# Kernel tuning notes

Measured on AMD Instinct MI355X. Metric: run time of the kernel, lower is better.

Reference implementation:

```python
import jax, jax.numpy as jnp
import numpy as np

A_DIM, V_DIM, L_DIM, H = 512, 768, 1024, 512
B, S = 16, 2048


def setup_inputs() -> dict:
    key = jax.random.key(0)
    ks = jax.random.split(key, 20)
    w = lambda k, shp: jax.random.normal(k, shp, dtype=jnp.float32) * 0.02
    return {
        "a_input": jax.random.normal(ks[0], (B, S, A_DIM), dtype=jnp.float32),
        "v_input": jax.random.normal(ks[1], (B, S, V_DIM), dtype=jnp.float32),
        "l_input": jax.random.normal(ks[2], (B, S, L_DIM), dtype=jnp.float32),
        "h0": jax.random.normal(ks[3], (1, B, H), dtype=jnp.float32),
        "c0": jax.random.normal(ks[4], (1, B, H), dtype=jnp.float32),
        # 1x1 Conv1d == per-timestep Linear: weight [H, in_dim], bias [H]
        "Wa": w(ks[5], (H, A_DIM)), "ba": w(ks[6], (H,)),
        "Wv": w(ks[7], (H, V_DIM)), "bv": w(ks[8], (H,)),
        "Wl": w(ks[9], (H, L_DIM)), "bl": w(ks[10], (H,)),
        "Wc": w(ks[11], (H, 3 * H)), "bc": w(ks[12], (H,)),
        # LSTM params, PyTorch gate order (i, f, g, o)
        "Wih": w(ks[13], (4 * H, H)), "Whh": w(ks[14], (4 * H, H)),
        "bih": w(ks[15], (4 * H,)), "bhh": w(ks[16], (4 * H,)),
    }


def _lstm(x, h0, c0, Wih, Whh, bih, bhh):
    # x: [B, S, H]; h0/c0: [B, H]
    def step(carry, xt):
        h, c = carry
        gates = xt @ Wih.T + bih + h @ Whh.T + bhh  # [B, 4H]
        i, f, g, o = jnp.split(gates, 4, axis=-1)
        c = jax.nn.sigmoid(f) * c + jax.nn.sigmoid(i) * jnp.tanh(g)
        h = jax.nn.sigmoid(o) * jnp.tanh(c)
        return (h, c), h
    (hT, cT), hs = jax.lax.scan(step, (h0, c0), x.transpose(1, 0, 2))
    return hs.transpose(1, 0, 2), hT, cT  # [B,S,H], [B,H], [B,H]


def reference(a_input, v_input, l_input, h0, c0, Wa, ba, Wv, bv, Wl, bl,
              Wc, bc, Wih, Whh, bih, bhh):
    # 1x1 conv projections -> [B, S, H]
    a = a_input @ Wa.T + ba
    v = v_input @ Wv.T + bv
    l = l_input @ Wl.T + bl
    # attention fusion
    context = jnp.tanh(jnp.concatenate([a, v, l], axis=-1) @ Wc.T + bc)  # [B,S,H]
    scores = jnp.stack([
        jnp.sum(a * context, axis=-1),
        jnp.sum(v * context, axis=-1),
        jnp.sum(l * context, axis=-1),
    ], axis=-1)  # [B, S, 3]
    weight = jax.nn.softmax(scores, axis=-1)[..., None]  # [B,S,3,1]
    data = jnp.stack([a, v, l], axis=-2)  # [B,S,3,H]
    fusion = jnp.sum(data * weight, axis=-2)  # [B,S,H]
    r_out, hT, cT = _lstm(fusion, h0[0], c0[0], Wih, Whh, bih, bhh)
    return r_out, hT[None], cT[None]
```

## Files before the change

kernel.cpp:

```cpp
#include <hip/hip_runtime.h>
#include <stdint.h>

#define B_ 16
#define S_ 2048
#define H_ 512
#define M_ (B_ * S_)

template <int ACT>
__global__ __launch_bounds__(256) void gemm_xwt(
    const float* __restrict__ X, const float* __restrict__ W,
    const float* __restrict__ b1, const float* __restrict__ b2,
    float* __restrict__ Y, int K, int ldy)
{
  __shared__ float As[16][132];
  __shared__ float Bs[16][132];
  const int tid = threadIdx.x;
  const int bm = blockIdx.x, bn = blockIdx.y;
  const int ty = tid >> 4, tx = tid & 15;
  const int lr = tid >> 2, lk = (tid & 3) << 2;
  const float* Xb = X + (size_t)(bm * 128) * K;
  const float* Wb = W + (size_t)(bn * 128) * K;

  float acc[8][8] = {};

  for (int k0 = 0; k0 < K; k0 += 16) {
    float4 xa0 = *(const float4*)(Xb + (size_t)lr * K + k0 + lk);
    float4 xa1 = *(const float4*)(Xb + (size_t)(lr + 64) * K + k0 + lk);
    float4 wa0 = *(const float4*)(Wb + (size_t)lr * K + k0 + lk);
    float4 wa1 = *(const float4*)(Wb + (size_t)(lr + 64) * K + k0 + lk);
    __syncthreads();
    As[lk + 0][lr] = xa0.x; As[lk + 1][lr] = xa0.y; As[lk + 2][lr] = xa0.z; As[lk + 3][lr] = xa0.w;
    As[lk + 0][lr + 64] = xa1.x; As[lk + 1][lr + 64] = xa1.y; As[lk + 2][lr + 64] = xa1.z; As[lk + 3][lr + 64] = xa1.w;
    Bs[lk + 0][lr] = wa0.x; Bs[lk + 1][lr] = wa0.y; Bs[lk + 2][lr] = wa0.z; Bs[lk + 3][lr] = wa0.w;
    Bs[lk + 0][lr + 64] = wa1.x; Bs[lk + 1][lr + 64] = wa1.y; Bs[lk + 2][lr + 64] = wa1.z; Bs[lk + 3][lr + 64] = wa1.w;
    __syncthreads();
#pragma unroll
    for (int kk = 0; kk < 16; ++kk) {
      float4 a0 = *(const float4*)&As[kk][ty * 8];
      float4 a1 = *(const float4*)&As[kk][ty * 8 + 4];
      float4 b0 = *(const float4*)&Bs[kk][tx * 8];
      float4 b1v = *(const float4*)&Bs[kk][tx * 8 + 4];
      float av[8] = {a0.x, a0.y, a0.z, a0.w, a1.x, a1.y, a1.z, a1.w};
      float bv[8] = {b0.x, b0.y, b0.z, b0.w, b1v.x, b1v.y, b1v.z, b1v.w};
#pragma unroll
      for (int i = 0; i < 8; ++i)
#pragma unroll
        for (int j = 0; j < 8; ++j) acc[i][j] += av[i] * bv[j];
    }
  }

  const int ncol0 = bn * 128 + tx * 8;
  float bias[8];
#pragma unroll
  for (int j = 0; j < 8; ++j) {
    float bb = b1[ncol0 + j];
    if (b2) bb += b2[ncol0 + j];
    bias[j] = bb;
  }
#pragma unroll
  for (int i = 0; i < 8; ++i) {
    size_t row = (size_t)bm * 128 + ty * 8 + i;
    float* yp = Y + row * (size_t)ldy + ncol0;
    float out[8];
#pragma unroll
    for (int j = 0; j < 8; ++j) {
      float v = acc[i][j] + bias[j];
      if (ACT) v = tanhf(v);
      out[j] = v;
    }
    *(float4*)(yp)     = make_float4(out[0], out[1], out[2], out[3]);
    *(float4*)(yp + 4) = make_float4(out[4], out[5], out[6], out[7]);
  }
}

__global__ __launch_bounds__(256) void fusion_kernel(
    const float* __restrict__ F,
    const float* __restrict__ CTX,
    float* __restrict__ FU)
{
  const int row = blockIdx.x * 4 + (threadIdx.x >> 6);
  const int lane = threadIdx.x & 63;
  const float* a = F + (size_t)row * 1536;
  const float* v = a + 512;
  const float* l = a + 1024;
  const float* c = CTX + (size_t)row * 512;
  float sa = 0.f, sv = 0.f, sl = 0.f;
  for (int k = lane; k < 512; k += 64) {
    float cv = c[k];
    sa += a[k] * cv; sv += v[k] * cv; sl += l[k] * cv;
  }
#pragma unroll
  for (int off = 1; off < 64; off <<= 1) {
    sa += __shfl_xor(sa, off);
    sv += __shfl_xor(sv, off);
    sl += __shfl_xor(sl, off);
  }
  float m = fmaxf(sa, fmaxf(sv, sl));
  float ea = expf(sa - m), ev = expf(sv - m), el = expf(sl - m);
  float inv = 1.0f / (ea + ev + el);
  float wa = ea * inv, wv = ev * inv, wl = el * inv;
  float* fu = FU + (size_t)row * 512;
  for (int k = lane; k < 512; k += 64)
    fu[k] = wa * a[k] + wv * v[k] + wl * l[k];
}

__device__ __forceinline__ float sigf(float x) { return 1.f / (1.f + expf(-x)); }
__device__ __forceinline__ float lo32f(unsigned long long w) {
  return __builtin_bit_cast(float, (unsigned int)w);
}

__global__ __launch_bounds__(256, 1) void lstm_kernel(
    const float* __restrict__ G,
    const float* __restrict__ Whh,
    const float* __restrict__ h0,
    const float* __restrict__ c0,
    unsigned long long* __restrict__ ring,
    unsigned long long* __restrict__ sent,
    float* __restrict__ r_out,
    float* __restrict__ hT,
    float* __restrict__ cT)
{
  const int bi = blockIdx.x;
  const int b  = ((bi & 7) << 1) | ((bi >> 3) & 1);
  const int wg = bi >> 4;
  const int k0h = wg << 5;
  const int tid = threadIdx.x;

  __shared__ float h_lds[2][512];
  __shared__ float gates_lds[128];
  __shared__ float c_lds[32];

  const int col = tid >> 1;
  const int khalf = tid & 1;
  const int kbase = khalf << 8;
  const int g = col >> 5, ul = col & 31;
  const int gcol = g * 512 + k0h + ul;

  float4 warr[64];
  const float* wsrc = Whh + (size_t)gcol * 512 + kbase;
#pragma unroll
  for (int j = 0; j < 64; ++j) warr[j] = *(const float4*)(wsrc + j * 4);

  const float* gbase = G + (size_t)b * S_ * 2048;

  if (tid < 32) c_lds[tid] = c0[b * H_ + k0h + tid];
  h_lds[0][tid]       = h0[b * H_ + tid];
  h_lds[0][tid + 256] = h0[b * H_ + tid + 256];
  float gval = (khalf == 0) ? gbase[gcol] : 0.f;
  __syncthreads();

  int buf = 0;
  for (int t = 0; t < S_; ++t) {
    const float* hb = &h_lds[buf][kbase];
    float4 s4 = make_float4(0.f, 0.f, 0.f, 0.f);
#pragma unroll
    for (int j = 0; j < 64; ++j) {
      float4 hv = *(const float4*)(hb + (j << 2));
      s4.x += warr[j].x * hv.x;
      s4.y += warr[j].y * hv.y;
      s4.z += warr[j].z * hv.z;
      s4.w += warr[j].w * hv.w;
    }
    float sum = (s4.x + s4.y) + (s4.z + s4.w);
    sum += __shfl_xor(sum, 1);
    if (khalf == 0) gates_lds[col] = sum + gval;
    __syncthreads();

    unsigned long long* slot = ring + ((size_t)(t & 3) * B_ + b) * H_;

    if (tid < 32) {
      const int u = tid;
      float ip = gates_lds[u], fp = gates_lds[32 + u];
      float gp = gates_lds[64 + u], op = gates_lds[96 + u];
      float ig = sigf(ip), fg = sigf(fp);
      float gg = tanhf(gp), og = sigf(op);
      float cn = fg * c_lds[u] + ig * gg;
      c_lds[u] = cn;
      float hn = og * tanhf(cn);
      unsigned long long pk =
          ((unsigned long long)(unsigned int)t << 32) |
          (unsigned long long)__builtin_bit_cast(unsigned int, hn);
      __hip_atomic_store(slot + k0h + u, pk, __ATOMIC_RELAXED,
                         __HIP_MEMORY_SCOPE_AGENT);
      if (u == 0) {
        __hip_atomic_store(sent + ((size_t)(t & 3) * B_ + b) * 16 + wg,
                           (unsigned long long)(unsigned int)t << 32,
                           __ATOMIC_RELAXED, __HIP_MEMORY_SCOPE_AGENT);
      }
      r_out[((size_t)b * S_ + t) * H_ + k0h + u] = hn;
      if (t == S_ - 1) {
        hT[b * H_ + k0h + u] = hn;
        cT[b * H_ + k0h + u] = cn;
      }
    }

    if (t + 1 < S_) {
      if (tid < 16) {
        const unsigned long long* sp =
            sent + ((size_t)(t & 3) * B_ + b) * 16 + tid;
        unsigned int got;
        do {
          got = (unsigned int)(__hip_atomic_load(sp, __ATOMIC_RELAXED,
                                                 __HIP_MEMORY_SCOPE_AGENT) >> 32);
        } while (got != (unsigned int)t);
      }
      __syncthreads();

      const unsigned int want = (unsigned int)t;
      unsigned long long v0 = __hip_atomic_load(slot + tid, __ATOMIC_RELAXED,
                                                __HIP_MEMORY_SCOPE_AGENT);
      unsigned long long v1 = __hip_atomic_load(slot + tid + 256, __ATOMIC_RELAXED,
                                                __HIP_MEMORY_SCOPE_AGENT);
      while ((((unsigned int)(v0 >> 32)) ^ want) |
             (((unsigned int)(v1 >> 32)) ^ want)) {
        v0 = __hip_atomic_load(slot + tid, __ATOMIC_RELAXED,
                               __HIP_MEMORY_SCOPE_AGENT);
        v1 = __hip_atomic_load(slot + tid + 256, __ATOMIC_RELAXED,
                               __HIP_MEMORY_SCOPE_AGENT);
      }
      h_lds[buf ^ 1][tid]       = lo32f(v0);
      h_lds[buf ^ 1][tid + 256] = lo32f(v1);

      if (khalf == 0) gval = gbase[(size_t)(t + 1) * 2048 + gcol];
      __syncthreads();
      buf ^= 1;
    }
  }
}

extern "C" void kernel_launch(void* const* d_in, const int* in_sizes, int n_in,
                              void* d_out, int out_size, void* d_ws, size_t ws_size,
                              hipStream_t stream)
{
  const float* a_in = (const float*)d_in[0];
  const float* v_in = (const float*)d_in[1];
  const float* l_in = (const float*)d_in[2];
  const float* h0   = (const float*)d_in[3];
  const float* c0   = (const float*)d_in[4];
  const float* Wa = (const float*)d_in[5];   const float* ba = (const float*)d_in[6];
  const float* Wv = (const float*)d_in[7];   const float* bv = (const float*)d_in[8];
  const float* Wl = (const float*)d_in[9];   const float* bl = (const float*)d_in[10];
  const float* Wc = (const float*)d_in[11];  const float* bc = (const float*)d_in[12];
  const float* Wih = (const float*)d_in[13]; const float* Whh = (const float*)d_in[14];
  const float* bih = (const float*)d_in[15]; const float* bhh = (const float*)d_in[16];

  char* ws = (char*)d_ws;
  float* Fbuf = (float*)ws;
  float* Gbuf = (float*)ws;
  float* CTX  = (float*)(ws + 268435456ull);
  float* FU   = (float*)(ws + 335544320ull);
  unsigned long long* ringp = (unsigned long long*)(ws + 402653184ull);
  unsigned long long* sentp = (unsigned long long*)(ws + 402653184ull + 262144ull);

  dim3 blk(256);
  gemm_xwt<0><<<dim3(256, 4), blk, 0, stream>>>(a_in, Wa, ba, nullptr, Fbuf + 0,    512,  1536);
  gemm_xwt<0><<<dim3(256, 4), blk, 0, stream>>>(v_in, Wv, bv, nullptr, Fbuf + 512,  768,  1536);
  gemm_xwt<0><<<dim3(256, 4), blk, 0, stream>>>(l_in, Wl, bl, nullptr, Fbuf + 1024, 1024, 1536);
  gemm_xwt<1><<<dim3(256, 4), blk, 0, stream>>>(Fbuf, Wc, bc, nullptr, CTX, 1536, 512);
  fusion_kernel<<<dim3(8192), blk, 0, stream>>>(Fbuf, CTX, FU);
  gemm_xwt<0><<<dim3(256, 16), blk, 0, stream>>>(FU, Wih, bih, bhh, Gbuf, 512, 2048);
  float* out = (float*)d_out;
  lstm_kernel<<<dim3(256), blk, 0, stream>>>(Gbuf, Whh, h0, c0, ringp, sentp,
                                             out, out + 16777216ull,
                                             out + 16777216ull + 8192ull);
}
```

Measured before the change: 10.50 ms.

## Duplicate LSTM h-exchange ring into workgroup-scope and agent-scope copies for faster polling

The cross-block hidden-state exchange now writes each h value and sent flag twice: once with workgroup-scope atomics, meant to reach the local L2 without bypassing caches, and once with agent-scope atomics. Consumers poll mostly the workgroup-scope copy (fetch_add of 0 or loads after a threadfence) and fall back to the agent-scope copy every fourth iteration. The aim is lower latency in the per-timestep spin-wait that serialises the 2048-step recurrence. The cost is doubled stores plus extra fences, and correctness relies on cache-coherence behaviour that workgroup scope does not guarantee across XCDs.

Result: slower. 40.45 ms (+285.4%).

```diff
diff --git a/kernel.cpp b/kernel.cpp
--- a/kernel.cpp
+++ b/kernel.cpp
@@ -114,8 +114,10 @@
     const float* __restrict__ Whh,
     const float* __restrict__ h0,
     const float* __restrict__ c0,
-    unsigned long long* __restrict__ ring,
-    unsigned long long* __restrict__ sent,
+    unsigned long long* __restrict__ ringL2,
+    unsigned long long* __restrict__ ringIF,
+    unsigned long long* __restrict__ sentL2,
+    unsigned long long* __restrict__ sentIF,
     float* __restrict__ r_out,
     float* __restrict__ hT,
     float* __restrict__ cT)
@@ -166,7 +168,9 @@
     if (khalf == 0) gates_lds[col] = sum + gval;
     __syncthreads();
 
-    unsigned long long* slot = ring + ((size_t)(t & 3) * B_ + b) * H_;
+    const size_t roff = ((size_t)(t & 3) * B_ + b) * H_;
+    unsigned long long* slotL2 = ringL2 + roff;
+    unsigned long long* slotIF = ringIF + roff;
 
     if (tid < 32) {
       const int u = tid;
@@ -180,12 +184,17 @@
       unsigned long long pk =
           ((unsigned long long)(unsigned int)t << 32) |
           (unsigned long long)__builtin_bit_cast(unsigned int, hn);
-      __hip_atomic_store(slot + k0h + u, pk, __ATOMIC_RELAXED,
+      __hip_atomic_store(slotL2 + k0h + u, pk, __ATOMIC_RELAXED,
+                         __HIP_MEMORY_SCOPE_WORKGROUP);
+      __hip_atomic_store(slotIF + k0h + u, pk, __ATOMIC_RELAXED,
                          __HIP_MEMORY_SCOPE_AGENT);
       if (u == 0) {
-        __hip_atomic_store(sent + ((size_t)(t & 3) * B_ + b) * 16 + wg,
-                           (unsigned long long)(unsigned int)t << 32,
-                           __ATOMIC_RELAXED, __HIP_MEMORY_SCOPE_AGENT);
+        const size_t so = ((size_t)(t & 3) * B_ + b) * 16 + wg;
+        const unsigned long long tagw = (unsigned long long)(unsigned int)t << 32;
+        __hip_atomic_store(sentL2 + so, tagw, __ATOMIC_RELAXED,
+                           __HIP_MEMORY_SCOPE_WORKGROUP);
+        __hip_atomic_store(sentIF + so, tagw, __ATOMIC_RELAXED,
+                           __HIP_MEMORY_SCOPE_AGENT);
       }
       r_out[((size_t)b * S_ + t) * H_ + k0h + u] = hn;
       if (t == S_ - 1) {
@@ -196,27 +205,48 @@
 
     if (t + 1 < S_) {
       if (tid < 16) {
-        const unsigned long long* sp =
-            sent + ((size_t)(t & 3) * B_ + b) * 16 + tid;
-        unsigned int got;
-        do {
-          got = (unsigned int)(__hip_atomic_load(sp, __ATOMIC_RELAXED,
-                                                 __HIP_MEMORY_SCOPE_AGENT) >> 32);
-        } while (got != (unsigned int)t);
+        const size_t so = ((size_t)(t & 3) * B_ + b) * 16 + tid;
+        const unsigned int want = (unsigned int)t;
+        for (int it = 0;; ++it) {
+          unsigned long long w;
+          if ((it & 3) != 3) {
+            w = __hip_atomic_fetch_add(sentL2 + so, 0ull, __ATOMIC_RELAXED,
+                                       __HIP_MEMORY_SCOPE_WORKGROUP);
+          } else {
+            w = __hip_atomic_load(sentIF + so, __ATOMIC_RELAXED,
+                                  __HIP_MEMORY_SCOPE_AGENT);
+          }
+          if ((unsigned int)(w >> 32) == want) break;
+        }
       }
       __syncthreads();
 
+      __threadfence();
       const unsigned int want = (unsigned int)t;
-      unsigned long long v0 = __hip_atomic_load(slot + tid, __ATOMIC_RELAXED,
-                                                __HIP_MEMORY_SCOPE_AGENT);
-      unsigned long long v1 = __hip_atomic_load(slot + tid + 256, __ATOMIC_RELAXED,
-                                                __HIP_MEMORY_SCOPE_AGENT);
+      unsigned long long v0 = __hip_atomic_load(slotL2 + tid, __ATOMIC_RELAXED,
+                                                __HIP_MEMORY_SCOPE_WORKGROUP);
+      unsigned long long v1 = __hip_atomic_load(slotL2 + tid + 256, __ATOMIC_RELAXED,
+                                                __HIP_MEMORY_SCOPE_WORKGROUP);
+      int it = 0;
       while ((((unsigned int)(v0 >> 32)) ^ want) |
              (((unsigned int)(v1 >> 32)) ^ want)) {
-        v0 = __hip_atomic_load(slot + tid, __ATOMIC_RELAXED,
-                               __HIP_MEMORY_SCOPE_AGENT);
-        v1 = __hip_atomic_load(slot + tid + 256, __ATOMIC_RELAXED,
-                               __HIP_MEMORY_SCOPE_AGENT);
+        ++it;
+        if ((it & 3) == 3) {
+          if ((unsigned int)(v0 >> 32) != want)
+            v0 = __hip_atomic_load(slotIF + tid, __ATOMIC_RELAXED,
+                                   __HIP_MEMORY_SCOPE_AGENT);
+          if ((unsigned int)(v1 >> 32) != want)
+            v1 = __hip_atomic_load(slotIF + tid + 256, __ATOMIC_RELAXED,
+                                   __HIP_MEMORY_SCOPE_AGENT);
+        } else {
+          __threadfence();
+          if ((unsigned int)(v0 >> 32) != want)
+            v0 = __hip_atomic_load(slotL2 + tid, __ATOMIC_RELAXED,
+                                   __HIP_MEMORY_SCOPE_WORKGROUP);
+          if ((unsigned int)(v1 >> 32) != want)
+            v1 = __hip_atomic_load(slotL2 + tid + 256, __ATOMIC_RELAXED,
+                                   __HIP_MEMORY_SCOPE_WORKGROUP);
+        }
       }
       h_lds[buf ^ 1][tid]       = lo32f(v0);
       h_lds[buf ^ 1][tid + 256] = lo32f(v1);
@@ -249,8 +279,10 @@
   float* Gbuf = (float*)ws;
   float* CTX  = (float*)(ws + 268435456ull);
   float* FU   = (float*)(ws + 335544320ull);
-  unsigned long long* ringp = (unsigned long long*)(ws + 402653184ull);
-  unsigned long long* sentp = (unsigned long long*)(ws + 402653184ull + 262144ull);
+  unsigned long long* ringL2 = (unsigned long long*)(ws + 402653184ull);
+  unsigned long long* ringIF = (unsigned long long*)(ws + 402653184ull + 262144ull);
+  unsigned long long* sentL2 = (unsigned long long*)(ws + 402653184ull + 524288ull);
+  unsigned long long* sentIF = (unsigned long long*)(ws + 402653184ull + 532480ull);
 
   dim3 blk(256);
   gemm_xwt<0><<<dim3(256, 4), blk, 0, stream>>>(a_in, Wa, ba, nullptr, Fbuf + 0,    512,  1536);
@@ -260,7 +292,8 @@
   fusion_kernel<<<dim3(8192), blk, 0, stream>>>(Fbuf, CTX, FU);
   gemm_xwt<0><<<dim3(256, 16), blk, 0, stream>>>(FU, Wih, bih, bhh, Gbuf, 512, 2048);
   float* out = (float*)d_out;
-  lstm_kernel<<<dim3(256), blk, 0, stream>>>(Gbuf, Whh, h0, c0, ringp, sentp,
+  lstm_kernel<<<dim3(256), blk, 0, stream>>>(Gbuf, Whh, h0, c0,
+                                             ringL2, ringIF, sentL2, sentIF,
                                              out, out + 16777216ull,
                                              out + 16777216ull + 8192ull);
 }
```

## Drop sentinel flags in LSTM sync and re-tile recurrent matvec per thread

Applied to the files above, without the earlier changes.

Removes the separate per-workgroup sentinel flag store and spin, relying only on the tagged h values in the ring buffer for cross-block synchronization. This drops one barrier and one global polling round per timestep. The recurrent matvec is also re-partitioned so each thread computes 4 gate rows over a 64-wide K slice, with rotated indexing to spread LDS bank accesses and an 8-lane shuffle reduction. Each thread now spins directly on its two ring slots, which may raise polling traffic on the ring.

Measured after the change: 8.997 ms. -14.3%, faster.

```diff
diff --git a/kernel.cpp b/kernel.cpp
--- a/kernel.cpp
+++ b/kernel.cpp
@@ -115,7 +115,6 @@
     const float* __restrict__ h0,
     const float* __restrict__ c0,
     unsigned long long* __restrict__ ring,
-    unsigned long long* __restrict__ sent,
     float* __restrict__ r_out,
     float* __restrict__ hT,
     float* __restrict__ cT)
@@ -130,40 +129,61 @@
   __shared__ float gates_lds[128];
   __shared__ float c_lds[32];
 
-  const int col = tid >> 1;
-  const int khalf = tid & 1;
-  const int kbase = khalf << 8;
-  const int g = col >> 5, ul = col & 31;
-  const int gcol = g * 512 + k0h + ul;
-
-  float4 warr[64];
-  const float* wsrc = Whh + (size_t)gcol * 512 + kbase;
-#pragma unroll
-  for (int j = 0; j < 64; ++j) warr[j] = *(const float4*)(wsrc + j * 4);
+  const int grp = tid >> 3;
+  const int j   = tid & 7;
+  const int lr0 = grp << 2;
+  const int grow0 = ((lr0 >> 5) << 9) + k0h + (lr0 & 31);
+
+  float4 wq[4][16];
+#pragma unroll
+  for (int i = 0; i < 16; ++i) {
+    const int m = (i + j) & 15;
+#pragma unroll
+    for (int r = 0; r < 4; ++r)
+      wq[r][i] = *(const float4*)(Whh + (size_t)(grow0 + r) * 512 + j * 64 + m * 4);
+  }
 
   const float* gbase = G + (size_t)b * S_ * 2048;
 
   if (tid < 32) c_lds[tid] = c0[b * H_ + k0h + tid];
   h_lds[0][tid]       = h0[b * H_ + tid];
   h_lds[0][tid + 256] = h0[b * H_ + tid + 256];
-  float gval = (khalf == 0) ? gbase[gcol] : 0.f;
+  float gval = (j < 4) ? gbase[grow0 + j] : 0.f;
   __syncthreads();
 
   int buf = 0;
   for (int t = 0; t < S_; ++t) {
-    const float* hb = &h_lds[buf][kbase];
-    float4 s4 = make_float4(0.f, 0.f, 0.f, 0.f);
-#pragma unroll
-    for (int j = 0; j < 64; ++j) {
-      float4 hv = *(const float4*)(hb + (j << 2));
-      s4.x += warr[j].x * hv.x;
-      s4.y += warr[j].y * hv.y;
-      s4.z += warr[j].z * hv.z;
-      s4.w += warr[j].w * hv.w;
-    }
-    float sum = (s4.x + s4.y) + (s4.z + s4.w);
-    sum += __shfl_xor(sum, 1);
-    if (khalf == 0) gates_lds[col] = sum + gval;
+    const float* hb = &h_lds[buf][j << 6];
+    float4 a0 = make_float4(0.f, 0.f, 0.f, 0.f);
+    float4 a1 = a0, a2 = a0, a3 = a0;
+#pragma unroll
+    for (int i = 0; i < 16; ++i) {
+      const int m = (i + j) & 15;
+      float4 hv = *(const float4*)(hb + (m << 2));
+      a0.x += wq[0][i].x * hv.x; a0.y += wq[0][i].y * hv.y;
+      a0.z += wq[0][i].z * hv.z; a0.w += wq[0][i].w * hv.w;
+      a1.x += wq[1][i].x * hv.x; a1.y += wq[1][i].y * hv.y;
+      a1.z += wq[1][i].z * hv.z; a1.w += wq[1][i].w * hv.w;
+      a2.x += wq[2][i].x * hv.x; a2.y += wq[2][i].y * hv.y;
+      a2.z += wq[2][i].z * hv.z; a2.w += wq[2][i].w * hv.w;
+      a3.x += wq[3][i].x * hv.x; a3.y += wq[3][i].y * hv.y;
+      a3.z += wq[3][i].z * hv.z; a3.w += wq[3][i].w * hv.w;
+    }
+    float s0 = (a0.x + a0.y) + (a0.z + a0.w);
+    float s1 = (a1.x + a1.y) + (a1.z + a1.w);
+    float s2 = (a2.x + a2.y) + (a2.z + a2.w);
+    float s3 = (a3.x + a3.y) + (a3.z + a3.w);
+#pragma unroll
+    for (int off = 1; off < 8; off <<= 1) {
+      s0 += __shfl_xor(s0, off);
+      s1 += __shfl_xor(s1, off);
+      s2 += __shfl_xor(s2, off);
+      s3 += __shfl_xor(s3, off);
+    }
+    if (j < 4) {
+      float sv = (j == 0) ? s0 : (j == 1) ? s1 : (j == 2) ? s2 : s3;
+      gates_lds[lr0 + j] = sv + gval;
+    }
     __syncthreads();
 
     unsigned long long* slot = ring + ((size_t)(t & 3) * B_ + b) * H_;
@@ -182,11 +202,6 @@
           (unsigned long long)__builtin_bit_cast(unsigned int, hn);
       __hip_atomic_store(slot + k0h + u, pk, __ATOMIC_RELAXED,
                          __HIP_MEMORY_SCOPE_AGENT);
-      if (u == 0) {
-        __hip_atomic_store(sent + ((size_t)(t & 3) * B_ + b) * 16 + wg,
-                           (unsigned long long)(unsigned int)t << 32,
-                           __ATOMIC_RELAXED, __HIP_MEMORY_SCOPE_AGENT);
-      }
       r_out[((size_t)b * S_ + t) * H_ + k0h + u] = hn;
       if (t == S_ - 1) {
         hT[b * H_ + k0h + u] = hn;
@@ -195,33 +210,20 @@
     }
 
     if (t + 1 < S_) {
-      if (tid < 16) {
-        const unsigned long long* sp =
-            sent + ((size_t)(t & 3) * B_ + b) * 16 + tid;
-        unsigned int got;
-        do {
-          got = (unsigned int)(__hip_atomic_load(sp, __ATOMIC_RELAXED,
-                                                 __HIP_MEMORY_SCOPE_AGENT) >> 32);
-        } while (got != (unsigned int)t);
-      }
-      __syncthreads();
-
       const unsigned int want = (unsigned int)t;
-      unsigned long long v0 = __hip_atomic_load(slot + tid, __ATOMIC_RELAXED,
-                                                __HIP_MEMORY_SCOPE_AGENT);
-      unsigned long long v1 = __hip_atomic_load(slot + tid + 256, __ATOMIC_RELAXED,
-                                                __HIP_MEMORY_SCOPE_AGENT);
-      while ((((unsigned int)(v0 >> 32)) ^ want) |
-             (((unsigned int)(v1 >> 32)) ^ want)) {
+      unsigned long long v0, v1;
+      for (;;) {
         v0 = __hip_atomic_load(slot + tid, __ATOMIC_RELAXED,
                                __HIP_MEMORY_SCOPE_AGENT);
         v1 = __hip_atomic_load(slot + tid + 256, __ATOMIC_RELAXED,
                                __HIP_MEMORY_SCOPE_AGENT);
+        if (!(((unsigned int)(v0 >> 32) ^ want) |
+              ((unsigned int)(v1 >> 32) ^ want))) break;
       }
       h_lds[buf ^ 1][tid]       = lo32f(v0);
       h_lds[buf ^ 1][tid + 256] = lo32f(v1);
 
-      if (khalf == 0) gval = gbase[(size_t)(t + 1) * 2048 + gcol];
+      if (j < 4) gval = gbase[(size_t)(t + 1) * 2048 + grow0 + j];
       __syncthreads();
       buf ^= 1;
     }
@@ -250,7 +252,6 @@
   float* CTX  = (float*)(ws + 268435456ull);
   float* FU   = (float*)(ws + 335544320ull);
   unsigned long long* ringp = (unsigned long long*)(ws + 402653184ull);
-  unsigned long long* sentp = (unsigned long long*)(ws + 402653184ull + 262144ull);
 
   dim3 blk(256);
   gemm_xwt<0><<<dim3(256, 4), blk, 0, stream>>>(a_in, Wa, ba, nullptr, Fbuf + 0,    512,  1536);
@@ -260,7 +261,7 @@
   fusion_kernel<<<dim3(8192), blk, 0, stream>>>(Fbuf, CTX, FU);
   gemm_xwt<0><<<dim3(256, 16), blk, 0, stream>>>(FU, Wih, bih, bhh, Gbuf, 512, 2048);
   float* out = (float*)d_out;
-  lstm_kernel<<<dim3(256), blk, 0, stream>>>(Gbuf, Whh, h0, c0, ringp, sentp,
+  lstm_kernel<<<dim3(256), blk, 0, stream>>>(Gbuf, Whh, h0, c0, ringp,
                                              out, out + 16777216ull,
                                              out + 16777216ull + 8192ull);
 }
```
